# Kernel optimization log

Hardware: AMD Instinct MI355X
Metric: run time of the kernel (lower is better)

Reference implementation:

```python
import jax, jax.numpy as jnp
import numpy as np

ALPHA = 100.0   # norse SuperSpike surrogate-gradient sharpness (default)
DT = 0.001      # norse LIFBoxParameters default dt

@jax.custom_vjp
def heaviside(x):
    # spike function with SuperSpike surrogate gradient (norse method='super')
    return (x > 0).astype(x.dtype)

def _hs_fwd(x):
    return (x > 0).astype(x.dtype), x

def _hs_bwd(x, g):
    return (g / (ALPHA * jnp.abs(x) + 1.0) ** 2,)

heaviside.defvjp(_hs_fwd, _hs_bwd)


def setup_inputs() -> dict:
    key = jax.random.key(0)
    k0, k1, k2, k3, k4 = jax.random.split(key, 5)
    B, F, T = 256, 10, 8192
    inputs = jax.random.normal(k0, (B, F, T), dtype=jnp.float32)
    # learned scalar LIF parameters (one per parallel temporal layer)
    tau = jnp.array([200.0, 300.0, 600.0], dtype=jnp.float32)   # tau_mem_inv
    v_th = jnp.array([0.006, 0.008, 0.013], dtype=jnp.float32)  # thresholds
    conv_w = jax.random.normal(k1, (1, 3, 1, 1), dtype=jnp.float32) * 0.5
    conv_b = jax.random.normal(k2, (1,), dtype=jnp.float32) * 0.1
    lin_w = jax.random.normal(k3, (2, 10), dtype=jnp.float32) * 0.3
    lin_b = jax.random.normal(k4, (2,), dtype=jnp.float32) * 0.1
    return {"inputs": inputs, "tau": tau, "v_th": v_th,
            "conv_w": conv_w, "conv_b": conv_b, "lin_w": lin_w, "lin_b": lin_b}


def reference(inputs, tau, v_th, conv_w, conv_b, lin_w, lin_b):
    # inputs: [B, F, T]
    B, F, T = inputs.shape
    x_t = jnp.transpose(inputs, (2, 0, 1))          # [T, B, F], time-major
    tau3 = tau[:, None, None]                        # [3,1,1] broadcast over B,F
    vth3 = v_th[:, None, None]
    v0 = jnp.zeros((3, B, F), dtype=inputs.dtype)    # v_leak = 0 initial state

    def step(v, x):
        # LIFBox dynamics: dv = dt * tau_inv * (v_leak - v + i), v_leak=v_reset=0
        v = v + DT * tau3 * (x[None, :, :] - v)      # [3,B,F]
        z = heaviside(v - vth3)                      # spikes
        v = (1.0 - z) * v                            # reset to v_reset=0 on spike
        return v, z

    _, zs = jax.lax.scan(step, v0, x_t)              # zs: [T, 3, B, F]
    resp = jnp.transpose(zs, (2, 1, 3, 0))           # [B, 3, F, T]

    # 1x1 Conv2d over the 3 LIF channels -> [B, F, T]
    conv = jnp.einsum('bcft,c->bft', resp, conv_w[0, :, 0, 0]) + conv_b[0]
    # Linear over feature dim F=10 -> 2, output [B, 2, T]
    out = jnp.einsum('bft,of->bot', conv, lin_w) + lin_b[None, :, None]
    return out
```

## Files before the change

kernel.cpp:

```cpp
#include <hip/hip_runtime.h>


#define T_LEN 8192
#define NF 10
#define NSEQ 30
#define CHUNK 256
#define WARM 128
#define NCHUNKS 32
#define CPB 4
#define GRIDY (NCHUNKS / CPB)

__device__ __forceinline__ float lif_step(float xx, float v, float k, float vt, bool& s) {
  float d  = __fsub_rn(xx, v);
  float p  = __fmul_rn(k, d);
  float vn = __fadd_rn(v, p);
  s = vn > vt;
  return s ? 0.0f : vn;
}

__device__ __forceinline__ void warm16(const float4 q0[4], const float4 q1[4],
                                       float& v0, float& v1, float k, float vt) {
#pragma unroll
  for (int i = 0; i < 4; ++i) {
    float x0[4] = {q0[i].x, q0[i].y, q0[i].z, q0[i].w};
    float x1[4] = {q1[i].x, q1[i].y, q1[i].z, q1[i].w};
#pragma unroll
    for (int r = 0; r < 4; ++r) {
      bool s0, s1;
      v0 = lif_step(x0[r], v0, k, vt, s0);
      v1 = lif_step(x1[r], v1, k, vt, s1);
    }
  }
}

__device__ __forceinline__ void main16(const float4 q0[4], const float4 q1[4],
                                       float& v0, float& v1, float k, float vt,
                                       int tt, int baseT,
                                       unsigned& m0, unsigned& m1,
                                       unsigned& m2, unsigned& m3) {
#pragma unroll
  for (int i = 0; i < 4; ++i) {
    float x0[4] = {q0[i].x, q0[i].y, q0[i].z, q0[i].w};
    float x1[4] = {q1[i].x, q1[i].y, q1[i].z, q1[i].w};
#pragma unroll
    for (int r = 0; r < 4; ++r) {
      bool s0, s1;
      v0 = lif_step(x0[r], v0, k, vt, s0);
      v1 = lif_step(x1[r], v1, k, vt, s1);
      unsigned long long ub0 = __ballot(s0);
      unsigned long long ub1 = __ballot(s1);
      const int t = baseT + i * 4 + r;
      if (tt == t) {
        m0 = (unsigned)(ub0 & 0xffffffffull);
        m1 = (unsigned)(ub1 & 0xffffffffull);
        m2 = (unsigned)(ub0 >> 32);
        m3 = (unsigned)(ub1 >> 32);
      }
    }
  }
}

__device__ __forceinline__ float lut_sum(unsigned m, const float* lut, int o, float bias) {
  float acc = bias;
#pragma unroll
  for (int g = 0; g < 6; ++g) {
    unsigned val = (m >> (5 * g)) & 31u;
    acc += lut[(g * 2 + o) * 32 + val];
  }
  return acc;
}

__global__ __launch_bounds__(64, 2) void lif_chunked(
    const float* __restrict__ x,
    const float* __restrict__ tau,
    const float* __restrict__ vth,
    const float* __restrict__ convw,
    const float* __restrict__ convb,
    const float* __restrict__ linw,
    const float* __restrict__ linb,
    float* __restrict__ out)
{
  const int b    = blockIdx.x;
  const int cb   = blockIdx.y;
  const int lane = threadIdx.x;
  const int half = lane >> 5;
  const int j    = lane & 31;
  const bool active = j < NSEQ;
  const int c = active ? j / NF : 0;
  const int f = active ? j % NF : 0;

  __shared__ float lut[384];
#pragma unroll
  for (int e = 0; e < 6; ++e) {
    int id = lane + 64 * e;
    int g = id >> 6, rem = id & 63, oo = rem >> 5, val = rem & 31;
    float sacc = 0.0f;
#pragma unroll
    for (int p = 0; p < 5; ++p) {
      if (val & (1 << p)) {
        int jj = 5 * g + p;
        sacc += convw[jj / NF] * linw[oo * NF + (jj % NF)];
      }
    }
    lut[id] = sacc;
  }
  __syncthreads();

  const float k  = __fmul_rn(0.001f, tau[c]);
  const float vt = active ? vth[c] : 3.0e38f;

  const int cBase = cb * CPB;
  const int myc0  = cBase + 2 * half;
  const int myc1  = myc0 + 1;
  const int t0_0  = myc0 * CHUNK;
  const int t0_1  = myc1 * CHUNK;
  const int ts0   = (myc0 == 0) ? 0 : (t0_0 - WARM);
  const int ts1   = t0_1 - WARM;

  const float* xrow = x + ((size_t)b * NF + f) * (size_t)T_LEN;
  const float4* pw0 = (const float4*)(xrow + ts0);
  const float4* pw1 = (const float4*)(xrow + ts1);
  const float4* pm0 = (const float4*)(xrow + t0_0);
  const float4* pm1 = (const float4*)(xrow + t0_1);

  const int o  = half;
  const int tt = j;
  float wsum = 0.0f;
#pragma unroll
  for (int f2 = 0; f2 < NF; ++f2) wsum += linw[o * NF + f2];
  const float bias = linb[o] + convb[0] * wsum;

  float* ob = out + ((size_t)b * 2 + o) * T_LEN + cBase * CHUNK + tt;

  float v0 = 0.0f, v1 = 0.0f;
  float4 a0[4], a1[4], b0[4], b1[4];
#pragma unroll
  for (int i = 0; i < 4; ++i) { a0[i] = pw0[i]; a1[i] = pw1[i]; }

#pragma unroll 1
  for (int sb = 0; sb < 8; sb += 2) {
#pragma unroll
    for (int i = 0; i < 4; ++i) {
      b0[i] = pw0[(sb + 1) * 4 + i];
      b1[i] = pw1[(sb + 1) * 4 + i];
    }
    warm16(a0, a1, v0, v1, k, vt);
    {
      const float4* n0 = (sb + 2 < 8) ? (pw0 + (sb + 2) * 4) : pm0;
      const float4* n1 = (sb + 2 < 8) ? (pw1 + (sb + 2) * 4) : pm1;
#pragma unroll
      for (int i = 0; i < 4; ++i) { a0[i] = n0[i]; a1[i] = n1[i]; }
    }
    warm16(b0, b1, v0, v1, k, vt);
  }
  v0 = (myc0 == 0) ? 0.0f : v0;

  unsigned m0 = 0, m1 = 0, m2 = 0, m3 = 0;
#pragma unroll 1
  for (int w = 0; w < 8; ++w) {
#pragma unroll
    for (int i = 0; i < 4; ++i) {
      b0[i] = pm0[(2 * w + 1) * 4 + i];
      b1[i] = pm1[(2 * w + 1) * 4 + i];
    }
    main16(a0, a1, v0, v1, k, vt, tt, 0, m0, m1, m2, m3);
    if (w < 7) {
#pragma unroll
      for (int i = 0; i < 4; ++i) {
        a0[i] = pm0[(2 * w + 2) * 4 + i];
        a1[i] = pm1[(2 * w + 2) * 4 + i];
      }
    }
    main16(b0, b1, v0, v1, k, vt, tt, 16, m0, m1, m2, m3);

    ob[w * 32            ] = lut_sum(m0, lut, o, bias);
    ob[w * 32 + 1 * CHUNK] = lut_sum(m1, lut, o, bias);
    ob[w * 32 + 2 * CHUNK] = lut_sum(m2, lut, o, bias);
    ob[w * 32 + 3 * CHUNK] = lut_sum(m3, lut, o, bias);
  }
}

extern "C" void kernel_launch(void* const* d_in, const int* in_sizes, int n_in,
                              void* d_out, int out_size, void* d_ws, size_t ws_size,
                              hipStream_t stream) {
  const float* x     = (const float*)d_in[0];
  const float* tau   = (const float*)d_in[1];
  const float* vthp  = (const float*)d_in[2];
  const float* convw = (const float*)d_in[3];
  const float* convb = (const float*)d_in[4];
  const float* linw  = (const float*)d_in[5];
  const float* linb  = (const float*)d_in[6];
  float* out = (float*)d_out;

  const int B = in_sizes[0] / (NF * T_LEN);
  lif_chunked<<<dim3(B, GRIDY), dim3(64), 0, stream>>>(
      x, tau, vthp, convw, convb, linw, linb, out);
}
```

Baseline: 160.8 us.

## Stage input tiles through double-buffered swizzled LDS with coalesced cooperative loads

Replaces per-lane strided float4 global loads, where each lane walks its own time row, with a cooperative scheme. The block loads contiguous 128-byte segments per stream into a double-buffered shared-memory tile using an XOR swizzle, and lanes then read their sequence from LDS. The aim is to coalesce global memory accesses and overlap the next stage's fetch with the current recurrence compute. The cost is a __syncthreads per 32-step stage plus extra LDS traffic and register pressure.

```diff
diff --git a/kernel.cpp b/kernel.cpp
--- a/kernel.cpp
+++ b/kernel.cpp
@@ -9,6 +9,9 @@
 #define NCHUNKS 32
 #define CPB 4
 #define GRIDY (NCHUNKS / CPB)
+#define NSTAGE 12
+#define FSTRIDE 36
+#define LDSW (CPB * NF * FSTRIDE)
 
 __device__ __forceinline__ float lif_step(float xx, float v, float k, float vt, bool& s) {
   float d  = __fsub_rn(xx, v);
@@ -16,48 +19,6 @@
   float vn = __fadd_rn(v, p);
   s = vn > vt;
   return s ? 0.0f : vn;
-}
-
-__device__ __forceinline__ void warm16(const float4 q0[4], const float4 q1[4],
-                                       float& v0, float& v1, float k, float vt) {
-#pragma unroll
-  for (int i = 0; i < 4; ++i) {
-    float x0[4] = {q0[i].x, q0[i].y, q0[i].z, q0[i].w};
-    float x1[4] = {q1[i].x, q1[i].y, q1[i].z, q1[i].w};
-#pragma unroll
-    for (int r = 0; r < 4; ++r) {
-      bool s0, s1;
-      v0 = lif_step(x0[r], v0, k, vt, s0);
-      v1 = lif_step(x1[r], v1, k, vt, s1);
-    }
-  }
-}
-
-__device__ __forceinline__ void main16(const float4 q0[4], const float4 q1[4],
-                                       float& v0, float& v1, float k, float vt,
-                                       int tt, int baseT,
-                                       unsigned& m0, unsigned& m1,
-                                       unsigned& m2, unsigned& m3) {
-#pragma unroll
-  for (int i = 0; i < 4; ++i) {
-    float x0[4] = {q0[i].x, q0[i].y, q0[i].z, q0[i].w};
-    float x1[4] = {q1[i].x, q1[i].y, q1[i].z, q1[i].w};
-#pragma unroll
-    for (int r = 0; r < 4; ++r) {
-      bool s0, s1;
-      v0 = lif_step(x0[r], v0, k, vt, s0);
-      v1 = lif_step(x1[r], v1, k, vt, s1);
-      unsigned long long ub0 = __ballot(s0);
-      unsigned long long ub1 = __ballot(s1);
-      const int t = baseT + i * 4 + r;
-      if (tt == t) {
-        m0 = (unsigned)(ub0 & 0xffffffffull);
-        m1 = (unsigned)(ub1 & 0xffffffffull);
-        m2 = (unsigned)(ub0 >> 32);
-        m3 = (unsigned)(ub1 >> 32);
-      }
-    }
-  }
 }
 
 __device__ __forceinline__ float lut_sum(unsigned m, const float* lut, int o, float bias) {
@@ -88,8 +49,11 @@
   const bool active = j < NSEQ;
   const int c = active ? j / NF : 0;
   const int f = active ? j % NF : 0;
-
+  const int fx = f & 7;
+
+  __shared__ __align__(16) float xs[2 * LDSW];
   __shared__ float lut[384];
+
 #pragma unroll
   for (int e = 0; e < 6; ++e) {
     int id = lane + 64 * e;
@@ -104,24 +68,28 @@
     }
     lut[id] = sacc;
   }
-  __syncthreads();
 
   const float k  = __fmul_rn(0.001f, tau[c]);
   const float vt = active ? vth[c] : 3.0e38f;
-
   const int cBase = cb * CPB;
   const int myc0  = cBase + 2 * half;
-  const int myc1  = myc0 + 1;
-  const int t0_0  = myc0 * CHUNK;
-  const int t0_1  = myc1 * CHUNK;
-  const int ts0   = (myc0 == 0) ? 0 : (t0_0 - WARM);
-  const int ts1   = t0_1 - WARM;
-
-  const float* xrow = x + ((size_t)b * NF + f) * (size_t)T_LEN;
-  const float4* pw0 = (const float4*)(xrow + ts0);
-  const float4* pw1 = (const float4*)(xrow + ts1);
-  const float4* pm0 = (const float4*)(xrow + t0_0);
-  const float4* pm1 = (const float4*)(xrow + t0_1);
+
+  const float* gbase[5];
+  int ldsoff[5];
+  int Dl[5];
+#pragma unroll
+  for (int i = 0; i < 5; ++i) {
+    int P = i * 64 + lane;
+    int stream = P >> 3;
+    int t16 = P & 7;
+    int q  = stream / NF;
+    int fL = stream - q * NF;
+    int t0q = (cBase + q) * CHUNK;
+    int tsq = t0q - WARM; if (tsq < 0) tsq = 0;
+    Dl[i] = t0q - tsq;
+    gbase[i] = x + ((size_t)b * NF + fL) * (size_t)T_LEN + tsq + t16 * 4;
+    ldsoff[i] = (q * NF + fL) * FSTRIDE + ((t16 ^ (fL & 7)) << 2);
+  }
 
   const int o  = half;
   const int tt = j;
@@ -129,54 +97,103 @@
 #pragma unroll
   for (int f2 = 0; f2 < NF; ++f2) wsum += linw[o * NF + f2];
   const float bias = linb[o] + convb[0] * wsum;
-
   float* ob = out + ((size_t)b * 2 + o) * T_LEN + cBase * CHUNK + tt;
 
+  const int rbA = (2 * half * NF + f) * FSTRIDE;
+  const int rbB = rbA + NF * FSTRIDE;
+
   float v0 = 0.0f, v1 = 0.0f;
-  float4 a0[4], a1[4], b0[4], b1[4];
-#pragma unroll
-  for (int i = 0; i < 4; ++i) { a0[i] = pw0[i]; a1[i] = pw1[i]; }
+
+  {
+    float4 tmp[5];
+#pragma unroll
+    for (int i = 0; i < 5; ++i) tmp[i] = *(const float4*)(gbase[i]);
+#pragma unroll
+    for (int i = 0; i < 5; ++i) *(float4*)(xs + ldsoff[i]) = tmp[i];
+  }
+  __syncthreads();
 
 #pragma unroll 1
-  for (int sb = 0; sb < 8; sb += 2) {
-#pragma unroll
-    for (int i = 0; i < 4; ++i) {
-      b0[i] = pw0[(sb + 1) * 4 + i];
-      b1[i] = pw1[(sb + 1) * 4 + i];
-    }
-    warm16(a0, a1, v0, v1, k, vt);
-    {
-      const float4* n0 = (sb + 2 < 8) ? (pw0 + (sb + 2) * 4) : pm0;
-      const float4* n1 = (sb + 2 < 8) ? (pw1 + (sb + 2) * 4) : pm1;
-#pragma unroll
-      for (int i = 0; i < 4; ++i) { a0[i] = n0[i]; a1[i] = n1[i]; }
-    }
-    warm16(b0, b1, v0, v1, k, vt);
-  }
+  for (int s = 0; s < 4; ++s) {
+    const int buf = s & 1;
+    const int sn = s + 1;
+    float4 tmp[5];
+#pragma unroll
+    for (int i = 0; i < 5; ++i) {
+      int off = (sn < 4) ? sn * 32 : (Dl[i] + (sn - 4) * 32);
+      tmp[i] = *(const float4*)(gbase[i] + off);
+    }
+    const float* baseA = xs + buf * LDSW + rbA;
+    const float* baseB = xs + buf * LDSW + rbB;
+#pragma unroll
+    for (int g = 0; g < 8; ++g) {
+      float4 qa = *(const float4*)(baseA + ((g ^ fx) << 2));
+      float4 qb = *(const float4*)(baseB + ((g ^ fx) << 2));
+      float xa[4] = {qa.x, qa.y, qa.z, qa.w};
+      float xb[4] = {qb.x, qb.y, qb.z, qb.w};
+#pragma unroll
+      for (int r = 0; r < 4; ++r) {
+        bool s0, s1;
+        v0 = lif_step(xa[r], v0, k, vt, s0);
+        v1 = lif_step(xb[r], v1, k, vt, s1);
+      }
+    }
+    const int nb = sn & 1;
+#pragma unroll
+    for (int i = 0; i < 5; ++i) *(float4*)(xs + nb * LDSW + ldsoff[i]) = tmp[i];
+    __syncthreads();
+  }
+
   v0 = (myc0 == 0) ? 0.0f : v0;
 
-  unsigned m0 = 0, m1 = 0, m2 = 0, m3 = 0;
 #pragma unroll 1
-  for (int w = 0; w < 8; ++w) {
-#pragma unroll
-    for (int i = 0; i < 4; ++i) {
-      b0[i] = pm0[(2 * w + 1) * 4 + i];
-      b1[i] = pm1[(2 * w + 1) * 4 + i];
-    }
-    main16(a0, a1, v0, v1, k, vt, tt, 0, m0, m1, m2, m3);
-    if (w < 7) {
-#pragma unroll
-      for (int i = 0; i < 4; ++i) {
-        a0[i] = pm0[(2 * w + 2) * 4 + i];
-        a1[i] = pm1[(2 * w + 2) * 4 + i];
-      }
-    }
-    main16(b0, b1, v0, v1, k, vt, tt, 16, m0, m1, m2, m3);
-
+  for (int s = 4; s < NSTAGE; ++s) {
+    const int buf = s & 1;
+    const bool pf = (s + 1 < NSTAGE);
+    float4 tmp[5];
+    if (pf) {
+#pragma unroll
+      for (int i = 0; i < 5; ++i) {
+        int off = Dl[i] + (s + 1 - 4) * 32;
+        tmp[i] = *(const float4*)(gbase[i] + off);
+      }
+    }
+    const float* baseA = xs + buf * LDSW + rbA;
+    const float* baseB = xs + buf * LDSW + rbB;
+    unsigned m0 = 0, m1 = 0, m2 = 0, m3 = 0;
+#pragma unroll
+    for (int g = 0; g < 8; ++g) {
+      float4 qa = *(const float4*)(baseA + ((g ^ fx) << 2));
+      float4 qb = *(const float4*)(baseB + ((g ^ fx) << 2));
+      float xa[4] = {qa.x, qa.y, qa.z, qa.w};
+      float xb[4] = {qb.x, qb.y, qb.z, qb.w};
+#pragma unroll
+      for (int r = 0; r < 4; ++r) {
+        bool s0, s1;
+        v0 = lif_step(xa[r], v0, k, vt, s0);
+        v1 = lif_step(xb[r], v1, k, vt, s1);
+        unsigned long long ub0 = __ballot(s0);
+        unsigned long long ub1 = __ballot(s1);
+        const int t = g * 4 + r;
+        if (tt == t) {
+          m0 = (unsigned)(ub0 & 0xffffffffull);
+          m1 = (unsigned)(ub1 & 0xffffffffull);
+          m2 = (unsigned)(ub0 >> 32);
+          m3 = (unsigned)(ub1 >> 32);
+        }
+      }
+    }
+    const int w = s - 4;
     ob[w * 32            ] = lut_sum(m0, lut, o, bias);
     ob[w * 32 + 1 * CHUNK] = lut_sum(m1, lut, o, bias);
     ob[w * 32 + 2 * CHUNK] = lut_sum(m2, lut, o, bias);
     ob[w * 32 + 3 * CHUNK] = lut_sum(m3, lut, o, bias);
+    if (pf) {
+      const int nb = (s + 1) & 1;
+#pragma unroll
+      for (int i = 0; i < 5; ++i) *(float4*)(xs + nb * LDSW + ldsoff[i]) = tmp[i];
+    }
+    __syncthreads();
   }
 }
 
```

Result: no change. 162.6 us (+1.1%).
